# Performance work log

Hardware: AMD Instinct MI355X
Metric: run time of the kernel (lower is better)

The kernel has to match this reference:

```python
import jax, jax.numpy as jnp
import numpy as np

N = 100000      # nodes
E = 1600000     # edges (avg degree 16)
IN = 128        # input_dim
HID = 32        # hidden_dim per head (layer 1)
HEADS = 2       # heads (layer 1)
OUT = 32        # output_dim (layer 2, heads=1)
NEG_SLOPE = 0.2 # PyG GATConv default leaky relu slope


def setup_inputs() -> dict:
    key = jax.random.key(0)
    ks = jax.random.split(key, 10)
    s = 0.1  # glorot-ish scale
    x = jax.random.normal(ks[0], (N, IN), jnp.float32)
    edge_index = jax.random.randint(ks[1], (2, E), 0, N, dtype=jnp.int64)
    W1 = jax.random.normal(ks[2], (IN, HEADS * HID), jnp.float32) * s
    a1_src = jax.random.normal(ks[3], (HEADS, HID), jnp.float32) * s
    a1_dst = jax.random.normal(ks[4], (HEADS, HID), jnp.float32) * s
    b1 = jnp.zeros((HEADS * HID,), jnp.float32)
    W2 = jax.random.normal(ks[5], (HEADS * HID, OUT), jnp.float32) * s
    a2_src = jax.random.normal(ks[6], (1, OUT), jnp.float32) * s
    a2_dst = jax.random.normal(ks[7], (1, OUT), jnp.float32) * s
    b2 = jnp.zeros((OUT,), jnp.float32)
    return {"x": x, "edge_index": edge_index, "W1": W1, "a1_src": a1_src,
            "a1_dst": a1_dst, "b1": b1, "W2": W2, "a2_src": a2_src,
            "a2_dst": a2_dst, "b2": b2}


def _gat_layer(x, src, dst, W, a_src, a_dst, b, heads, out_ch, concat, n_nodes):
    # linear projection: [N, heads, out_ch]
    h = (x @ W).reshape(n_nodes, heads, out_ch)
    # per-node attention halves: [N, heads]
    alpha_s = jnp.einsum('nhc,hc->nh', h, a_src)
    alpha_d = jnp.einsum('nhc,hc->nh', h, a_dst)
    # per-edge raw score (message x_j = source node, softmax over dst segment)
    e = jax.nn.leaky_relu(alpha_s[src] + alpha_d[dst], NEG_SLOPE)  # [E, heads]
    # segment softmax over incoming edges of each dst node
    m = jax.ops.segment_max(e, dst, num_segments=n_nodes)          # [N, heads]
    m = jax.lax.stop_gradient(m)
    ee = jnp.exp(e - m[dst])
    denom = jax.ops.segment_sum(ee, dst, num_segments=n_nodes)     # [N, heads]
    alpha = ee / (denom[dst] + 1e-16)                              # [E, heads]
    # weighted scatter-add aggregation
    msg = h[src] * alpha[:, :, None]                               # [E, heads, out_ch]
    out = jax.ops.segment_sum(msg, dst, num_segments=n_nodes)      # [N, heads, out_ch]
    if concat:
        out = out.reshape(n_nodes, heads * out_ch)
    else:
        out = out.mean(axis=1)
    return out + b


def reference(x, edge_index, W1, a1_src, a1_dst, b1, W2, a2_src, a2_dst, b2):
    n = x.shape[0]
    # PyG GATConv adds self-loops by default (both layers, same edge set)
    loop = jnp.arange(n, dtype=edge_index.dtype)
    src = jnp.concatenate([edge_index[0], loop])
    dst = jnp.concatenate([edge_index[1], loop])
    h = _gat_layer(x, src, dst, W1, a1_src, a1_dst, b1, HEADS, HID, True, n)
    h = jax.nn.elu(h)
    return _gat_layer(h, src, dst, W2, a2_src, a2_dst, b2, 1, OUT, False, n)
```

## Files before the change

kernel.cpp:

```cpp
#include <hip/hip_runtime.h>
#include <math.h>

#define N_NODES 100000
#define N_EDGES 1600000
#define IN_DIM  128
#define C1      64
#define OUT_DIM 32
#define NEG_SLOPE 0.2f
#define LOG2E 1.44269504f

#define BSHIFT  8
#define BNODES  256
#define NBUCK   ((N_NODES + BNODES - 1) / BNODES)
#define CAP     5120
#define SLOTS   48
#define GC_STRIDE 16
#define G1_BLOCKS ((N_NODES + 127) / 128)

typedef _Float16 half8 __attribute__((ext_vector_type(8)));
typedef float    f32x4 __attribute__((ext_vector_type(4)));

__device__ __forceinline__ float wexp2(float sc) {
    return __builtin_amdgcn_exp2f(fmaxf(sc, NEG_SLOPE * sc));
}


__global__ void zero_k(int4* __restrict__ p, int n4) {
    int i = blockIdx.x * 256 + threadIdx.x;
    if (i < n4) p[i] = make_int4(0, 0, 0, 0);
}

__global__ __launch_bounds__(1024) void binp1_k(const int* __restrict__ ei,
        int* __restrict__ gcur, int* __restrict__ buf) {
    __shared__ int scnt[NBUCK], sbase[NBUCK], soff[NBUCK];
    int t = threadIdx.x;
    if (t < NBUCK) { scnt[t] = 0; soff[t] = 0; }
    __syncthreads();
    int  s[16], bk[16], ld[16];
    bool v[16];
    #pragma unroll
    for (int i = 0; i < 16; ++i) {
        int e = blockIdx.x * 16384 + i * 1024 + t;
        v[i] = e < N_EDGES;
        int ec = v[i] ? e : 0;
        s[i] = ei[ec];
        int d = ei[N_EDGES + ec];
        bk[i] = d >> BSHIFT;
        ld[i] = d & (BNODES - 1);
        if (v[i]) atomicAdd(&scnt[bk[i]], 1);
    }
    __syncthreads();
    if (t < NBUCK) sbase[t] = atomicAdd(&gcur[t * GC_STRIDE], scnt[t]);
    __syncthreads();
    #pragma unroll
    for (int i = 0; i < 16; ++i) {
        if (v[i]) {
            int p = sbase[bk[i]] + atomicAdd(&soff[bk[i]], 1);
            if (p < CAP) buf[bk[i] * CAP + p] = s[i] | (ld[i] << 17);
        }
    }
}

__global__ __launch_bounds__(256) void binp2_k(const int* __restrict__ gcur,
        const int* __restrict__ buf, int* __restrict__ csr, int* __restrict__ deg) {
    __shared__ int4 lcsr4[BNODES * SLOTS / 4];
    __shared__ int  lcnt[BNODES];
    int* lcsr = (int*)lcsr4;
    int b = blockIdx.x, t = threadIdx.x;
    lcnt[t] = 0;
    __syncthreads();
    int cnt = gcur[b * GC_STRIDE];
    if (cnt > CAP) cnt = CAP;
    const int* bb = buf + b * CAP;
    for (int e = t; e < cnt; e += 256) {
        int vv = bb[e];
        int src = vv & 0x1FFFF;
        int l = vv >> 17;
        int slot = atomicAdd(&lcnt[l], 1);
        if (slot < SLOTS) lcsr[l * SLOTS + slot] = src;
    }
    __syncthreads();
    int4* g4 = (int4*)csr + (size_t)b * (BNODES * SLOTS / 4);
    #pragma unroll
    for (int i = 0; i < BNODES * SLOTS / 4 / 256; ++i)
        g4[t + i * 256] = lcsr4[t + i * 256];
    int c = lcnt[t];
    deg[b * BNODES + t] = c < SLOTS ? c : SLOTS;
}

__global__ void prep_k(const float* __restrict__ W1, const float* __restrict__ W2,
                       _Float16* __restrict__ w1t, _Float16* __restrict__ w2t) {
    int t = blockIdx.x * 256 + threadIdx.x;
    if (t < IN_DIM * C1) {
        int k = t >> 6, n = t & 63;
        w1t[n * IN_DIM + k] = (_Float16)W1[t];
    }
    if (t < C1 * OUT_DIM) {
        int k = t >> 5, n = t & 31;
        w2t[n * C1 + k] = (_Float16)W2[t];
    }
}

__global__ __launch_bounds__(256) void gemm1_k(const float* __restrict__ x,
        const _Float16* __restrict__ w1t, const float* __restrict__ a_s,
        const float* __restrict__ a_d, _Float16* __restrict__ h,
        float* __restrict__ as_o, float* __restrict__ ad_o) {
    __shared__ _Float16 sh[4][32 * 72];
    int t = threadIdx.x;
    int wv = t >> 6, lane = t & 63, m = lane & 15, q = lane >> 4;
    int rbw = blockIdx.x * 128 + wv * 32;
    f32x4 acc[2][4];
    #pragma unroll
    for (int i = 0; i < 2; ++i)
        #pragma unroll
        for (int j = 0; j < 4; ++j) acc[i][j] = (f32x4){0.f, 0.f, 0.f, 0.f};
    #pragma unroll
    for (int ks = 0; ks < 4; ++ks) {
        half8 a[2];
        #pragma unroll
        for (int rt = 0; rt < 2; ++rt) {
            int r = rbw + rt * 16 + m;
            r = r < N_NODES ? r : 0;
            const float4* p = (const float4*)(x + (size_t)r * IN_DIM + ks * 32 + q * 8);
            float4 f0 = p[0], f1 = p[1];
            half8 av;
            av[0] = (_Float16)f0.x; av[1] = (_Float16)f0.y;
            av[2] = (_Float16)f0.z; av[3] = (_Float16)f0.w;
            av[4] = (_Float16)f1.x; av[5] = (_Float16)f1.y;
            av[6] = (_Float16)f1.z; av[7] = (_Float16)f1.w;
            a[rt] = av;
        }
        #pragma unroll
        for (int ct = 0; ct < 4; ++ct) {
            half8 b = *(const half8*)(w1t + (ct * 16 + m) * IN_DIM + ks * 32 + q * 8);
            acc[0][ct] = __builtin_amdgcn_mfma_f32_16x16x32_f16(a[0], b, acc[0][ct], 0, 0, 0);
            acc[1][ct] = __builtin_amdgcn_mfma_f32_16x16x32_f16(a[1], b, acc[1][ct], 0, 0, 0);
        }
    }
    _Float16* ws = sh[wv];
    #pragma unroll
    for (int rt = 0; rt < 2; ++rt)
        #pragma unroll
        for (int ct = 0; ct < 4; ++ct)
            #pragma unroll
            for (int r = 0; r < 4; ++r)
                ws[(rt * 16 + q * 4 + r) * 72 + ct * 16 + m] = (_Float16)acc[rt][ct][r];
    __syncthreads();
    int rl = lane >> 1, hp = lane & 1;
    int rg = rbw + rl;
    if (rg < N_NODES) {
        float As_r[32], Ad_r[32];
        const float4* ap = (const float4*)(a_s + hp * 32);
        const float4* dp = (const float4*)(a_d + hp * 32);
        #pragma unroll
        for (int i = 0; i < 8; ++i) {
            float4 v = ap[i];
            As_r[4*i] = v.x; As_r[4*i+1] = v.y; As_r[4*i+2] = v.z; As_r[4*i+3] = v.w;
            float4 u = dp[i];
            Ad_r[4*i] = u.x; Ad_r[4*i+1] = u.y; Ad_r[4*i+2] = u.z; Ad_r[4*i+3] = u.w;
        }
        const _Float16* rowp = ws + rl * 72 + hp * 32;
        half8 c0 = *(const half8*)(rowp);
        half8 c1 = *(const half8*)(rowp + 8);
        half8 c2 = *(const half8*)(rowp + 16);
        half8 c3 = *(const half8*)(rowp + 24);
        float s = 0.f, dd = 0.f;
        #pragma unroll
        for (int j = 0; j < 8; ++j) {
            s  = fmaf((float)c0[j], As_r[j],      s);
            dd = fmaf((float)c0[j], Ad_r[j],      dd);
            s  = fmaf((float)c1[j], As_r[8 + j],  s);
            dd = fmaf((float)c1[j], Ad_r[8 + j],  dd);
            s  = fmaf((float)c2[j], As_r[16 + j], s);
            dd = fmaf((float)c2[j], Ad_r[16 + j], dd);
            s  = fmaf((float)c3[j], As_r[24 + j], s);
            dd = fmaf((float)c3[j], Ad_r[24 + j], dd);
        }
        as_o[rg * 2 + hp] = s  * LOG2E;
        ad_o[rg * 2 + hp] = dd * LOG2E;
        _Float16* hr = h + (size_t)rg * C1 + hp * 32;
        *(half8*)(hr)      = c0;
        *(half8*)(hr + 8)  = c1;
        *(half8*)(hr + 16) = c2;
        *(half8*)(hr + 24) = c3;
    }
}

__global__ __launch_bounds__(256) void agg1g2_k(const int* __restrict__ deg,
        const int* __restrict__ csr, const _Float16* __restrict__ h1,
        const float* __restrict__ as1, const float* __restrict__ ad1,
        const float* __restrict__ b1, const _Float16* __restrict__ w2t,
        const float* __restrict__ a2s, const float* __restrict__ a2d,
        _Float16* __restrict__ h2, float* __restrict__ as2o,
        float* __restrict__ ad2o) {
    __shared__ _Float16 shu[16 * 72];
    __shared__ _Float16 sh2[16 * 36];
    int t = threadIdx.x;
    int wv = t >> 6, lane = t & 63;
    int dl   = lane >> 4;
    int eg   = (lane >> 3) & 1;
    int cl   = lane & 7;
    int head = cl >> 2;
    int lr   = wv * 4 + dl;
    int d    = blockIdx.x * 16 + lr;

    int cnt = deg[d];
    const int* row = csr + d * SLOTS;
    float advl = ad1[d * 2 + head];
    float acc[8] = {0.f, 0.f, 0.f, 0.f, 0.f, 0.f, 0.f, 0.f};
    float wsum = 0.f;
    for (int base = 0; base < cnt; base += 4) {
        int e0 = base + eg, e1 = base + 2 + eg;
        bool v0 = e0 < cnt, v1 = e1 < cnt;
        int s0 = row[v0 ? e0 : 0];
        int s1 = row[v1 ? e1 : 0];
        float a0 = as1[(unsigned)(s0 * 2 + head)];
        float a1 = as1[(unsigned)(s1 * 2 + head)];
        half8 g0 = *(const half8*)(h1 + (unsigned)(s0 * C1 + 8 * cl));
        half8 g1 = *(const half8*)(h1 + (unsigned)(s1 * C1 + 8 * cl));
        float w0 = v0 ? wexp2(a0 + advl) : 0.f;
        float w1 = v1 ? wexp2(a1 + advl) : 0.f;
        #pragma unroll
        for (int i = 0; i < 8; ++i) {
            acc[i] = fmaf((float)g0[i], w0, acc[i]);
            acc[i] = fmaf((float)g1[i], w1, acc[i]);
        }
        wsum += w0 + w1;
    }
    if (eg == 0) {
        float w = wexp2(as1[d * 2 + head] + advl);
        half8 g = *(const half8*)(h1 + (unsigned)(d * C1 + 8 * cl));
        #pragma unroll
        for (int i = 0; i < 8; ++i) acc[i] = fmaf((float)g[i], w, acc[i]);
        wsum += w;
    }
    #pragma unroll
    for (int i = 0; i < 8; ++i) acc[i] += __shfl_xor(acc[i], 8);
    wsum += __shfl_xor(wsum, 8);
    if (eg == 0) {
        float inv = 1.f / (wsum + 1e-16f);
        const float4* bv = (const float4*)(b1 + 8 * cl);
        float o[8];
        #pragma unroll
        for (int i = 0; i < 4; ++i) {
            o[i]     = acc[i]     * inv + (&bv[0].x)[i];
            o[4 + i] = acc[4 + i] * inv + (&bv[1].x)[i];
        }
        half8 hv;
        #pragma unroll
        for (int i = 0; i < 8; ++i) {
            float e = o[i] > 0.f ? o[i] : __expf(o[i]) - 1.f;
            hv[i] = (_Float16)e;
        }
        *(half8*)(shu + lr * 72 + cl * 8) = hv;
    }
    __syncthreads();

    if (wv == 0) {
        int m = lane & 15, q = lane >> 4;
        f32x4 c2[2];
        c2[0] = (f32x4){0.f, 0.f, 0.f, 0.f};
        c2[1] = (f32x4){0.f, 0.f, 0.f, 0.f};
        #pragma unroll
        for (int ks = 0; ks < 2; ++ks) {
            half8 a = *(const half8*)(shu + m * 72 + ks * 32 + q * 8);
            #pragma unroll
            for (int ct = 0; ct < 2; ++ct) {
                half8 b = *(const half8*)(w2t + (ct * 16 + m) * C1 + ks * 32 + q * 8);
                c2[ct] = __builtin_amdgcn_mfma_f32_16x16x32_f16(a, b, c2[ct], 0, 0, 0);
            }
        }
        #pragma unroll
        for (int ct = 0; ct < 2; ++ct)
            #pragma unroll
            for (int r = 0; r < 4; ++r)
                sh2[(q * 4 + r) * 36 + ct * 16 + m] = (_Float16)c2[ct][r];
    }
    __syncthreads();

    if (wv == 0 && lane < 16) {
        int rg = blockIdx.x * 16 + lane;
        float As_r[32], Ad_r[32];
        const float4* ap = (const float4*)a2s;
        const float4* dp = (const float4*)a2d;
        #pragma unroll
        for (int i = 0; i < 8; ++i) {
            float4 v = ap[i];
            As_r[4*i] = v.x; As_r[4*i+1] = v.y; As_r[4*i+2] = v.z; As_r[4*i+3] = v.w;
            float4 u = dp[i];
            Ad_r[4*i] = u.x; Ad_r[4*i+1] = u.y; Ad_r[4*i+2] = u.z; Ad_r[4*i+3] = u.w;
        }
        const _Float16* rowp = sh2 + lane * 36;
        half8 c0 = *(const half8*)(rowp);
        half8 c1 = *(const half8*)(rowp + 8);
        half8 c2 = *(const half8*)(rowp + 16);
        half8 c3 = *(const half8*)(rowp + 24);
        float s = 0.f, dd = 0.f;
        #pragma unroll
        for (int j = 0; j < 8; ++j) {
            s  = fmaf((float)c0[j], As_r[j],      s);
            dd = fmaf((float)c0[j], Ad_r[j],      dd);
            s  = fmaf((float)c1[j], As_r[8 + j],  s);
            dd = fmaf((float)c1[j], Ad_r[8 + j],  dd);
            s  = fmaf((float)c2[j], As_r[16 + j], s);
            dd = fmaf((float)c2[j], Ad_r[16 + j], dd);
            s  = fmaf((float)c3[j], As_r[24 + j], s);
            dd = fmaf((float)c3[j], Ad_r[24 + j], dd);
        }
        as2o[rg] = s  * LOG2E;
        ad2o[rg] = dd * LOG2E;
        _Float16* hr = h2 + (size_t)rg * OUT_DIM;
        *(half8*)(hr)      = c0;
        *(half8*)(hr + 8)  = c1;
        *(half8*)(hr + 16) = c2;
        *(half8*)(hr + 24) = c3;
    }
}

__global__ __launch_bounds__(256) void agg2_k(const int* __restrict__ deg,
        const int* __restrict__ csr, const _Float16* __restrict__ h2,
        const float* __restrict__ as2, const float* __restrict__ ad2,
        const float* __restrict__ b2, float* __restrict__ out) {
    int lane = threadIdx.x & 63;
    int dl   = lane >> 3;
    int eg   = (lane >> 2) & 1;
    int cl   = lane & 3;
    int d = ((blockIdx.x * 256 + threadIdx.x) >> 6) * 8 + dl;
    int cnt = deg[d];
    const int* row = csr + d * SLOTS;
    float advl = ad2[d];
    float acc[8] = {0.f, 0.f, 0.f, 0.f, 0.f, 0.f, 0.f, 0.f};
    float wsum = 0.f;
    for (int base = 0; base < cnt; base += 4) {
        int e0 = base + eg, e1 = base + 2 + eg;
        bool v0 = e0 < cnt, v1 = e1 < cnt;
        int s0 = row[v0 ? e0 : 0];
        int s1 = row[v1 ? e1 : 0];
        float a0 = as2[(unsigned)s0];
        float a1 = as2[(unsigned)s1];
        half8 g0 = *(const half8*)(h2 + (unsigned)(s0 * OUT_DIM + 8 * cl));
        half8 g1 = *(const half8*)(h2 + (unsigned)(s1 * OUT_DIM + 8 * cl));
        float w0 = v0 ? wexp2(a0 + advl) : 0.f;
        float w1 = v1 ? wexp2(a1 + advl) : 0.f;
        #pragma unroll
        for (int i = 0; i < 8; ++i) {
            acc[i] = fmaf((float)g0[i], w0, acc[i]);
            acc[i] = fmaf((float)g1[i], w1, acc[i]);
        }
        wsum += w0 + w1;
    }
    if (eg == 0) {
        float w = wexp2(as2[d] + advl);
        half8 g = *(const half8*)(h2 + (unsigned)(d * OUT_DIM + 8 * cl));
        #pragma unroll
        for (int i = 0; i < 8; ++i) acc[i] = fmaf((float)g[i], w, acc[i]);
        wsum += w;
    }
    #pragma unroll
    for (int i = 0; i < 8; ++i) acc[i] += __shfl_xor(acc[i], 4);
    wsum += __shfl_xor(wsum, 4);
    if (eg == 0) {
        float inv = 1.f / (wsum + 1e-16f);
        const float4* bv = (const float4*)(b2 + 8 * cl);
        float4 o0, o1;
        o0.x = acc[0] * inv + bv[0].x; o0.y = acc[1] * inv + bv[0].y;
        o0.z = acc[2] * inv + bv[0].z; o0.w = acc[3] * inv + bv[0].w;
        o1.x = acc[4] * inv + bv[1].x; o1.y = acc[5] * inv + bv[1].y;
        o1.z = acc[6] * inv + bv[1].z; o1.w = acc[7] * inv + bv[1].w;
        float4* ow = (float4*)(out + (size_t)d * OUT_DIM + 8 * cl);
        ow[0] = o0;
        ow[1] = o1;
    }
}


extern "C" void kernel_launch(void* const* d_in, const int* in_sizes, int n_in,
                              void* d_out, int out_size, void* d_ws, size_t ws_size,
                              hipStream_t stream) {
    const float* x   = (const float*)d_in[0];
    const int*   ei  = (const int*)d_in[1];
    const float* W1  = (const float*)d_in[2];
    const float* a1s = (const float*)d_in[3];
    const float* a1d = (const float*)d_in[4];
    const float* b1  = (const float*)d_in[5];
    const float* W2  = (const float*)d_in[6];
    const float* a2s = (const float*)d_in[7];
    const float* a2d = (const float*)d_in[8];
    const float* b2  = (const float*)d_in[9];
    float* out = (float*)d_out;

    char* ws = (char*)d_ws;
    size_t off = 0;
    auto alloc = [&](size_t bytes) -> void* {
        void* p = ws + off;
        off = (off + bytes + 255) & ~(size_t)255;
        return p;
    };
    int* gcur      = (int*)alloc((size_t)NBUCK * GC_STRIDE * 4);
    int* buf       = (int*)alloc((size_t)NBUCK * CAP * 4);
    int* csr       = (int*)alloc((size_t)NBUCK * BNODES * SLOTS * 4);
    int* deg       = (int*)alloc((size_t)NBUCK * BNODES * 4);
    _Float16* w1t  = (_Float16*)alloc((size_t)IN_DIM * C1 * 2);
    _Float16* w2t  = (_Float16*)alloc((size_t)C1 * OUT_DIM * 2);
    _Float16* h1   = (_Float16*)alloc((size_t)N_NODES * C1 * 2);
    float* as1     = (float*)alloc((size_t)N_NODES * 2 * 4);
    float* ad1     = (float*)alloc((size_t)N_NODES * 2 * 4);
    _Float16* h2   = (_Float16*)alloc((size_t)N_NODES * OUT_DIM * 2);
    float* as2     = (float*)alloc((size_t)N_NODES * 4);
    float* ad2     = (float*)alloc((size_t)N_NODES * 4);

    const int ZN4 = NBUCK * GC_STRIDE / 4;
    zero_k<<<(ZN4 + 255) / 256, 256, 0, stream>>>((int4*)gcur, ZN4);
    binp1_k<<<(N_EDGES + 16383) / 16384, 1024, 0, stream>>>(ei, gcur, buf);
    binp2_k<<<NBUCK, 256, 0, stream>>>(gcur, buf, csr, deg);
    prep_k<<<(IN_DIM * C1 + 255) / 256, 256, 0, stream>>>(W1, W2, w1t, w2t);

    gemm1_k<<<G1_BLOCKS, 256, 0, stream>>>(x, w1t, a1s, a1d, h1, as1, ad1);
    agg1g2_k<<<N_NODES / 16, 256, 0, stream>>>(deg, csr, h1, as1, ad1, b1,
                                               w2t, a2s, a2d, h2, as2, ad2);
    agg2_k<<<N_NODES / 32, 256, 0, stream>>>(deg, csr, h2, as2, ad2, b2, out);
}
```

Before: 225.1 us.

## Fold self-loops into CSR, unroll gather loops 4-wide, parallelize layer-2 attention dot

The CSR build kernel now appends each node's self-loop as an extra CSR entry and bumps its degree, so the aggregation kernels no longer need a separate self-loop tail. Both aggregation loops process four edges per lane-pair per iteration instead of two, putting more independent gathers in flight. In the fused layer-1/layer-2 kernel, the final attention dot product is spread across all 64 lanes of wave 0 with shuffle reductions instead of 16 lanes, and one block barrier is replaced by an LDS wait plus early exit of the other waves. When a node's in-degree fills all slots, the self-loop overwrites the last neighbor slot. The wider unroll also raises register pressure.

```diff
diff --git a/kernel.cpp b/kernel.cpp
--- a/kernel.cpp
+++ b/kernel.cpp
@@ -80,12 +80,16 @@
         if (slot < SLOTS) lcsr[l * SLOTS + slot] = src;
     }
     __syncthreads();
+    int c = lcnt[t];
+    int slot = c < SLOTS ? c : SLOTS - 1;
+    lcsr[t * SLOTS + slot] = b * BNODES + t;
+    int cd = c + 1;
+    deg[b * BNODES + t] = cd < SLOTS ? cd : SLOTS;
+    __syncthreads();
     int4* g4 = (int4*)csr + (size_t)b * (BNODES * SLOTS / 4);
     #pragma unroll
     for (int i = 0; i < BNODES * SLOTS / 4 / 256; ++i)
         g4[t + i * 256] = lcsr4[t + i * 256];
-    int c = lcnt[t];
-    deg[b * BNODES + t] = c < SLOTS ? c : SLOTS;
 }
 
 __global__ void prep_k(const float* __restrict__ W1, const float* __restrict__ W2,
@@ -209,30 +213,33 @@
     float advl = ad1[d * 2 + head];
     float acc[8] = {0.f, 0.f, 0.f, 0.f, 0.f, 0.f, 0.f, 0.f};
     float wsum = 0.f;
-    for (int base = 0; base < cnt; base += 4) {
-        int e0 = base + eg, e1 = base + 2 + eg;
-        bool v0 = e0 < cnt, v1 = e1 < cnt;
+    for (int base = 0; base < cnt; base += 8) {
+        int e0 = base + eg, e1 = e0 + 2, e2 = e0 + 4, e3 = e0 + 6;
+        bool v0 = e0 < cnt, v1 = e1 < cnt, v2 = e2 < cnt, v3 = e3 < cnt;
         int s0 = row[v0 ? e0 : 0];
         int s1 = row[v1 ? e1 : 0];
+        int s2 = row[v2 ? e2 : 0];
+        int s3 = row[v3 ? e3 : 0];
         float a0 = as1[(unsigned)(s0 * 2 + head)];
         float a1 = as1[(unsigned)(s1 * 2 + head)];
+        float a2 = as1[(unsigned)(s2 * 2 + head)];
+        float a3 = as1[(unsigned)(s3 * 2 + head)];
         half8 g0 = *(const half8*)(h1 + (unsigned)(s0 * C1 + 8 * cl));
         half8 g1 = *(const half8*)(h1 + (unsigned)(s1 * C1 + 8 * cl));
+        half8 g2 = *(const half8*)(h1 + (unsigned)(s2 * C1 + 8 * cl));
+        half8 g3 = *(const half8*)(h1 + (unsigned)(s3 * C1 + 8 * cl));
         float w0 = v0 ? wexp2(a0 + advl) : 0.f;
         float w1 = v1 ? wexp2(a1 + advl) : 0.f;
+        float w2 = v2 ? wexp2(a2 + advl) : 0.f;
+        float w3 = v3 ? wexp2(a3 + advl) : 0.f;
         #pragma unroll
         for (int i = 0; i < 8; ++i) {
             acc[i] = fmaf((float)g0[i], w0, acc[i]);
             acc[i] = fmaf((float)g1[i], w1, acc[i]);
-        }
-        wsum += w0 + w1;
-    }
-    if (eg == 0) {
-        float w = wexp2(as1[d * 2 + head] + advl);
-        half8 g = *(const half8*)(h1 + (unsigned)(d * C1 + 8 * cl));
-        #pragma unroll
-        for (int i = 0; i < 8; ++i) acc[i] = fmaf((float)g[i], w, acc[i]);
-        wsum += w;
+            acc[i] = fmaf((float)g2[i], w2, acc[i]);
+            acc[i] = fmaf((float)g3[i], w3, acc[i]);
+        }
+        wsum += (w0 + w1) + (w2 + w3);
     }
     #pragma unroll
     for (int i = 0; i < 8; ++i) acc[i] += __shfl_xor(acc[i], 8);
@@ -255,8 +262,9 @@
         *(half8*)(shu + lr * 72 + cl * 8) = hv;
     }
     __syncthreads();
-
-    if (wv == 0) {
+    if (wv != 0) return;
+
+    {
         int m = lane & 15, q = lane >> 4;
         f32x4 c2[2];
         c2[0] = (f32x4){0.f, 0.f, 0.f, 0.f};
@@ -276,44 +284,31 @@
             for (int r = 0; r < 4; ++r)
                 sh2[(q * 4 + r) * 36 + ct * 16 + m] = (_Float16)c2[ct][r];
     }
-    __syncthreads();
-
-    if (wv == 0 && lane < 16) {
-        int rg = blockIdx.x * 16 + lane;
-        float As_r[32], Ad_r[32];
-        const float4* ap = (const float4*)a2s;
-        const float4* dp = (const float4*)a2d;
-        #pragma unroll
-        for (int i = 0; i < 8; ++i) {
-            float4 v = ap[i];
-            As_r[4*i] = v.x; As_r[4*i+1] = v.y; As_r[4*i+2] = v.z; As_r[4*i+3] = v.w;
-            float4 u = dp[i];
-            Ad_r[4*i] = u.x; Ad_r[4*i+1] = u.y; Ad_r[4*i+2] = u.z; Ad_r[4*i+3] = u.w;
-        }
-        const _Float16* rowp = sh2 + lane * 36;
-        half8 c0 = *(const half8*)(rowp);
-        half8 c1 = *(const half8*)(rowp + 8);
-        half8 c2 = *(const half8*)(rowp + 16);
-        half8 c3 = *(const half8*)(rowp + 24);
+    asm volatile("s_waitcnt lgkmcnt(0)" ::: "memory");
+
+    {
+        int r = lane & 15, p = lane >> 4;
+        int rg = blockIdx.x * 16 + r;
+        const float4* ap = (const float4*)(a2s + p * 8);
+        const float4* dp = (const float4*)(a2d + p * 8);
+        float4 av0 = ap[0], av1 = ap[1];
+        float4 dv0 = dp[0], dv1 = dp[1];
+        float As[8] = {av0.x, av0.y, av0.z, av0.w, av1.x, av1.y, av1.z, av1.w};
+        float Ad[8] = {dv0.x, dv0.y, dv0.z, dv0.w, dv1.x, dv1.y, dv1.z, dv1.w};
+        half8 c = *(const half8*)(sh2 + r * 36 + p * 8);
         float s = 0.f, dd = 0.f;
         #pragma unroll
         for (int j = 0; j < 8; ++j) {
-            s  = fmaf((float)c0[j], As_r[j],      s);
-            dd = fmaf((float)c0[j], Ad_r[j],      dd);
-            s  = fmaf((float)c1[j], As_r[8 + j],  s);
-            dd = fmaf((float)c1[j], Ad_r[8 + j],  dd);
-            s  = fmaf((float)c2[j], As_r[16 + j], s);
-            dd = fmaf((float)c2[j], Ad_r[16 + j], dd);
-            s  = fmaf((float)c3[j], As_r[24 + j], s);
-            dd = fmaf((float)c3[j], Ad_r[24 + j], dd);
-        }
-        as2o[rg] = s  * LOG2E;
-        ad2o[rg] = dd * LOG2E;
-        _Float16* hr = h2 + (size_t)rg * OUT_DIM;
-        *(half8*)(hr)      = c0;
-        *(half8*)(hr + 8)  = c1;
-        *(half8*)(hr + 16) = c2;
-        *(half8*)(hr + 24) = c3;
+            s  = fmaf((float)c[j], As[j], s);
+            dd = fmaf((float)c[j], Ad[j], dd);
+        }
+        s  += __shfl_xor(s, 16);  s  += __shfl_xor(s, 32);
+        dd += __shfl_xor(dd, 16); dd += __shfl_xor(dd, 32);
+        if (p == 0) {
+            as2o[rg] = s  * LOG2E;
+            ad2o[rg] = dd * LOG2E;
+        }
+        *(half8*)(h2 + (size_t)rg * OUT_DIM + p * 8) = c;
     }
 }
 
@@ -331,30 +326,33 @@
     float advl = ad2[d];
     float acc[8] = {0.f, 0.f, 0.f, 0.f, 0.f, 0.f, 0.f, 0.f};
     float wsum = 0.f;
-    for (int base = 0; base < cnt; base += 4) {
-        int e0 = base + eg, e1 = base + 2 + eg;
-        bool v0 = e0 < cnt, v1 = e1 < cnt;
+    for (int base = 0; base < cnt; base += 8) {
+        int e0 = base + eg, e1 = e0 + 2, e2 = e0 + 4, e3 = e0 + 6;
+        bool v0 = e0 < cnt, v1 = e1 < cnt, v2 = e2 < cnt, v3 = e3 < cnt;
         int s0 = row[v0 ? e0 : 0];
         int s1 = row[v1 ? e1 : 0];
+        int s2 = row[v2 ? e2 : 0];
+        int s3 = row[v3 ? e3 : 0];
         float a0 = as2[(unsigned)s0];
         float a1 = as2[(unsigned)s1];
+        float a2 = as2[(unsigned)s2];
+        float a3 = as2[(unsigned)s3];
         half8 g0 = *(const half8*)(h2 + (unsigned)(s0 * OUT_DIM + 8 * cl));
         half8 g1 = *(const half8*)(h2 + (unsigned)(s1 * OUT_DIM + 8 * cl));
+        half8 g2 = *(const half8*)(h2 + (unsigned)(s2 * OUT_DIM + 8 * cl));
+        half8 g3 = *(const half8*)(h2 + (unsigned)(s3 * OUT_DIM + 8 * cl));
         float w0 = v0 ? wexp2(a0 + advl) : 0.f;
         float w1 = v1 ? wexp2(a1 + advl) : 0.f;
+        float w2 = v2 ? wexp2(a2 + advl) : 0.f;
+        float w3 = v3 ? wexp2(a3 + advl) : 0.f;
         #pragma unroll
         for (int i = 0; i < 8; ++i) {
             acc[i] = fmaf((float)g0[i], w0, acc[i]);
             acc[i] = fmaf((float)g1[i], w1, acc[i]);
-        }
-        wsum += w0 + w1;
-    }
-    if (eg == 0) {
-        float w = wexp2(as2[d] + advl);
-        half8 g = *(const half8*)(h2 + (unsigned)(d * OUT_DIM + 8 * cl));
-        #pragma unroll
-        for (int i = 0; i < 8; ++i) acc[i] = fmaf((float)g[i], w, acc[i]);
-        wsum += w;
+            acc[i] = fmaf((float)g2[i], w2, acc[i]);
+            acc[i] = fmaf((float)g3[i], w3, acc[i]);
+        }
+        wsum += (w0 + w1) + (w2 + w3);
     }
     #pragma unroll
     for (int i = 0; i < 8; ++i) acc[i] += __shfl_xor(acc[i], 4);
```

Result: faster. 217.6 us (-3.4%).
